# Kernel tuning notes

Measured on AMD Instinct MI355X. Metric: run time of the kernel, lower is better.

Reference implementation:

```python
import jax, jax.numpy as jnp
import numpy as np

SR = 48000
SOUND_SPEED = 343.0
MAX_ORDER = 10
RIR_LEN = 24000
BETA = 0.9          # uniform wall reflection coefficient
TAPS = 81           # fractional-delay windowed-sinc length
HALF = TAPS // 2    # 40 taps each side; also the global RIR offset


def _axis_tables(max_order):
    # Allen-Berkley image indices per axis: coord = (1-2p)*src + 2n*L
    n = np.arange(-max_order, max_order + 1)            # [2N+1]
    p = np.array([0, 1])
    P, N = np.meshgrid(p, n, indexing='ij')             # [2, 2N+1]
    sign = (1 - 2 * P).ravel().astype(np.float32)       # +/-1
    off = (2 * N).ravel().astype(np.float32)
    order = (np.abs(N - P) + np.abs(N)).ravel().astype(np.float32)  # wall hits per axis
    return jnp.asarray(sign), jnp.asarray(off), jnp.asarray(order)  # each [42]


def setup_inputs() -> dict:
    key = jax.random.key(0)
    # fractions in (0.1, 0.9): avoids degenerate rooms / mic-on-wall
    x = 0.1 + 0.8 * jax.random.uniform(key, (8, 9), dtype=jnp.float32)
    return {"input": x}


def reference(input):
    room = input[:, 0:3] * 10.0                 # [B,3] room dimensions (m)
    mic = input[:, 3:6] * room                  # [B,3]
    src = input[:, 6:9] * room                  # [B,3]
    B = room.shape[0]

    sign, off, order = _axis_tables(MAX_ORDER)  # [A] each, A=42

    # per-axis image coordinate minus mic coordinate: [B,3,A]
    img = sign[None, None, :] * src[:, :, None] + off[None, None, :] * room[:, :, None]
    d = img - mic[:, :, None]

    # squared distance over 3-axis outer product -> [B,A,A,A] -> [B,I], I=A^3
    d2 = (d[:, 0, :, None, None] ** 2
          + d[:, 1, None, :, None] ** 2
          + d[:, 2, None, None, :] ** 2)
    dist = jnp.sqrt(d2).reshape(B, -1)                              # [B,I]

    tot_order = (order[:, None, None] + order[None, :, None]
                 + order[None, None, :]).reshape(-1)                # [I]
    keep = tot_order <= MAX_ORDER

    amp = jnp.where(keep[None, :],
                    (BETA ** tot_order)[None, :] / (4.0 * jnp.pi * dist),
                    0.0)                                            # [B,I]

    tau = SR * dist / SOUND_SPEED          # fractional delay in samples
    i0 = jnp.floor(tau)
    frac = tau - i0                        # [B,I] in [0,1)

    k = jnp.arange(TAPS, dtype=jnp.float32) - HALF                   # [T]
    t = k[None, None, :] - frac[:, :, None]                          # [B,I,T]
    win = jnp.where(jnp.abs(t) <= HALF,
                    0.5 * (1.0 + jnp.cos(jnp.pi * t / (HALF + 1))), 0.0)
    h = jnp.sinc(t) * win                                            # windowed sinc

    ki = jnp.arange(TAPS, dtype=jnp.int32)
    idx = i0.astype(jnp.int32)[:, :, None] + HALF + ki[None, None, :]  # [B,I,T]
    valid = (idx >= 0) & (idx < RIR_LEN)
    vals = amp[:, :, None] * h * valid

    bofs = (jnp.arange(B, dtype=jnp.int32) * RIR_LEN)[:, None, None]
    flat_idx = jnp.clip(idx, 0, RIR_LEN - 1) + bofs
    rir = (jnp.zeros(B * RIR_LEN, dtype=jnp.float32)
           .at[flat_idx.ravel()].add(vals.ravel())
           .reshape(B, RIR_LEN))

    origin = 40.0 + SR * jnp.linalg.norm(mic - src, axis=1) / SOUND_SPEED
    return rir, origin
```

## Files before the change

### kernel.cpp

```cpp
#include <hip/hip_runtime.h>
#include <math.h>

#define SRf 48000.0f
#define CSOUND 343.0f
#define RIR_LEN 24000
#define TAPS 81
#define HALFT 40
#define NB 8
#define NM 21
#define NTRIP (NM * NM * NM)
#define NSL 16
#define BLOCK 1024
#define CAPS 256

__device__ __constant__ float c_beta[11] = {
    1.0f, 0.9f, 0.81f, 0.729f, 0.6561f, 0.59049f, 0.531441f,
    0.4782969f, 0.43046721f, 0.387420489f, 0.3486784401f};

__device__ __forceinline__ void axis_entry(int m, float& sgn, float& off, int& ord) {
    if (m < 11) {
        int n = m - 5;
        sgn = 1.0f;
        off = 2.0f * (float)n;
        ord = 2 * abs(n);
    } else {
        int n = m - 15;
        sgn = -1.0f;
        off = 2.0f * (float)n;
        ord = abs(n - 1) + abs(n);
    }
}

__global__ __launch_bounds__(BLOCK) void k_paint(const float* __restrict__ x,
                                                 float* __restrict__ ws) {
    __shared__ __align__(16) float s_tile[RIR_LEN];
    __shared__ float4 s_e[CAPS];
    __shared__ int s_cnt;

    const float PIF = 3.14159265358979323846f;
    const int b = blockIdx.x >> 4;
    const int sl = blockIdx.x & (NSL - 1);
    const int tid = threadIdx.x;

    const float* xb = x + b * 9;
    const float r0 = xb[0] * 10.0f, r1 = xb[1] * 10.0f, r2 = xb[2] * 10.0f;
    const float m0 = xb[3] * r0, m1 = xb[4] * r1, m2 = xb[5] * r2;
    const float s0 = xb[6] * r0, s1 = xb[7] * r1, s2 = xb[8] * r2;

    if (tid == 0) s_cnt = 0;
    for (int j = tid * 4; j < RIR_LEN; j += BLOCK * 4)
        *(float4*)&s_tile[j] = make_float4(0.f, 0.f, 0.f, 0.f);
    __syncthreads();

    {
        int r = sl + tid * NSL;
        if (r < NTRIP) {
            int mi = r / (NM * NM);
            int rem = r - mi * (NM * NM);
            int mj = rem / NM;
            int mk = rem - mj * NM;

            float si, oi_; int qi; axis_entry(mi, si, oi_, qi);
            float sj, oj_; int qj; axis_entry(mj, sj, oj_, qj);
            float sk, ok_; int qk; axis_entry(mk, sk, ok_, qk);
            int q = qi + qj + qk;
            if (q <= 10) {
                float dx = si * s0 + oi_ * r0 - m0;
                float dy = sj * s1 + oj_ * r1 - m1;
                float dz = sk * s2 + ok_ * r2 - m2;
                float dist = sqrtf(dx * dx + dy * dy + dz * dz);

                float tau = SRf * dist / CSOUND;
                float i0f = floorf(tau);
                int i0 = (int)i0f;
                if (i0 + HALFT + 1 < RIR_LEN) {
                    float fr = tau - i0f;
                    float amp = c_beta[q] / (4.0f * PIF * dist);
                    int slot = atomicAdd(&s_cnt, 1);
                    float4 e;
                    e.x = amp;
                    e.y = fr;
                    e.z = amp * __sinf(PIF * fr) * (1.0f / PIF);
                    e.w = __int_as_float(i0);
                    s_e[slot] = e;
                }
            }
        }
    }
    __syncthreads();

    const int n = s_cnt;
    const int total = n * (TAPS - 1);
    for (int w = tid; w < total; w += BLOCK) {
        int img = w / (TAPS - 1);
        int ki = w - img * (TAPS - 1) + 1;
        float4 e = s_e[img];
        int idx = __float_as_int(e.w) + HALFT + ki;
        if (idx >= RIR_LEN) continue;

        float tt = (float)(ki - HALFT) - e.y;
        float win = 0.5f * (1.0f + __cosf(PIF * (1.0f / 41.0f) * tt));
        float v = ((ki & 1) ? e.z : -e.z) * __builtin_amdgcn_rcpf(tt);
        v = (tt == 0.0f) ? e.x : v;
        atomicAdd(&s_tile[idx], v * win);
    }
    __syncthreads();

    float* wb = ws + (size_t)(b * NSL + sl) * RIR_LEN;
    for (int j = tid * 4; j < RIR_LEN; j += BLOCK * 4)
        *(float4*)&wb[j] = *(const float4*)&s_tile[j];
}

__global__ __launch_bounds__(256) void k_reduce(const float* __restrict__ x,
                                                const float* __restrict__ ws,
                                                float* __restrict__ out) {
    int t4 = (blockIdx.x * 256 + threadIdx.x) * 4;
    if (t4 < NB * RIR_LEN) {
        int b = t4 / RIR_LEN;
        int j = t4 - b * RIR_LEN;
        const float* base = ws + (size_t)b * NSL * RIR_LEN + j;
        float4 acc = *(const float4*)base;
        #pragma unroll
        for (int s = 1; s < NSL; ++s) {
            float4 v = *(const float4*)(base + (size_t)s * RIR_LEN);
            acc.x += v.x; acc.y += v.y; acc.z += v.z; acc.w += v.w;
        }
        *(float4*)(out + t4) = acc;
    }
    if (blockIdx.x == 0 && threadIdx.x < NB) {
        const float* xb = x + threadIdx.x * 9;
        float r0 = xb[0] * 10.0f, r1 = xb[1] * 10.0f, r2 = xb[2] * 10.0f;
        float d0 = (xb[3] - xb[6]) * r0;
        float d1 = (xb[4] - xb[7]) * r1;
        float d2 = (xb[5] - xb[8]) * r2;
        float dist = sqrtf(d0 * d0 + d1 * d1 + d2 * d2);
        out[NB * RIR_LEN + threadIdx.x] = 40.0f + SRf * dist / CSOUND;
    }
}

extern "C" void kernel_launch(void* const* d_in, const int* in_sizes, int n_in,
                              void* d_out, int out_size, void* d_ws, size_t ws_size,
                              hipStream_t stream) {
    const float* x = (const float*)d_in[0];
    float* out = (float*)d_out;
    float* ws = (float*)d_ws;

    k_paint<<<NB * NSL, BLOCK, 0, stream>>>(x, ws);
    int rblocks = (NB * RIR_LEN / 4 + 255) / 256;
    k_reduce<<<rblocks, 256, 0, stream>>>(x, ws, out);
}
```

Measured before the change: 26.39 us.

## Fuse paint and reduce kernels via cooperative grid sync

Merges the per-slice painting kernel and the cross-slice reduction kernel into one cooperative kernel that uses a grid-wide barrier between phases. Each block then reduces a 1500-sample span of its batch's RIR across the 16 slice partials. This removes the second kernel launch and its gap. In exchange it pays for a grid barrier and cooperative-launch overhead, and it limits reduction parallelism to 128 blocks.

```diff
diff --git a/kernel.cpp b/kernel.cpp
--- a/kernel.cpp
+++ b/kernel.cpp
@@ -1,4 +1,5 @@
 #include <hip/hip_runtime.h>
+#include <hip/hip_cooperative_groups.h>
 #include <math.h>
 
 #define SRf 48000.0f
@@ -12,6 +13,9 @@
 #define NSL 16
 #define BLOCK 1024
 #define CAPS 256
+#define SPAN (RIR_LEN / NSL)
+
+namespace cg = cooperative_groups;
 
 __device__ __constant__ float c_beta[11] = {
     1.0f, 0.9f, 0.81f, 0.729f, 0.6561f, 0.59049f, 0.531441f,
@@ -31,8 +35,9 @@
     }
 }
 
-__global__ __launch_bounds__(BLOCK) void k_paint(const float* __restrict__ x,
-                                                 float* __restrict__ ws) {
+__global__ __launch_bounds__(BLOCK) void k_fused(const float* __restrict__ x,
+                                                 float* __restrict__ ws,
+                                                 float* __restrict__ out) {
     __shared__ __align__(16) float s_tile[RIR_LEN];
     __shared__ float4 s_e[CAPS];
     __shared__ int s_cnt;
@@ -109,32 +114,30 @@
     float* wb = ws + (size_t)(b * NSL + sl) * RIR_LEN;
     for (int j = tid * 4; j < RIR_LEN; j += BLOCK * 4)
         *(float4*)&wb[j] = *(const float4*)&s_tile[j];
-}
 
-__global__ __launch_bounds__(256) void k_reduce(const float* __restrict__ x,
-                                                const float* __restrict__ ws,
-                                                float* __restrict__ out) {
-    int t4 = (blockIdx.x * 256 + threadIdx.x) * 4;
-    if (t4 < NB * RIR_LEN) {
-        int b = t4 / RIR_LEN;
-        int j = t4 - b * RIR_LEN;
-        const float* base = ws + (size_t)b * NSL * RIR_LEN + j;
-        float4 acc = *(const float4*)base;
-        #pragma unroll
-        for (int s = 1; s < NSL; ++s) {
-            float4 v = *(const float4*)(base + (size_t)s * RIR_LEN);
-            acc.x += v.x; acc.y += v.y; acc.z += v.z; acc.w += v.w;
+    cg::this_grid().sync();
+
+    {
+        int j4 = sl * SPAN + tid * 4;
+        if (tid * 4 < SPAN) {
+            const float* base = ws + (size_t)b * NSL * RIR_LEN + j4;
+            float4 acc = *(const float4*)base;
+            #pragma unroll
+            for (int s = 1; s < NSL; ++s) {
+                float4 v = *(const float4*)(base + (size_t)s * RIR_LEN);
+                acc.x += v.x; acc.y += v.y; acc.z += v.z; acc.w += v.w;
+            }
+            *(float4*)(out + (size_t)b * RIR_LEN + j4) = acc;
         }
-        *(float4*)(out + t4) = acc;
-    }
-    if (blockIdx.x == 0 && threadIdx.x < NB) {
-        const float* xb = x + threadIdx.x * 9;
-        float r0 = xb[0] * 10.0f, r1 = xb[1] * 10.0f, r2 = xb[2] * 10.0f;
-        float d0 = (xb[3] - xb[6]) * r0;
-        float d1 = (xb[4] - xb[7]) * r1;
-        float d2 = (xb[5] - xb[8]) * r2;
-        float dist = sqrtf(d0 * d0 + d1 * d1 + d2 * d2);
-        out[NB * RIR_LEN + threadIdx.x] = 40.0f + SRf * dist / CSOUND;
+        if (blockIdx.x == 0 && tid < NB) {
+            const float* xo = x + tid * 9;
+            float q0 = xo[0] * 10.0f, q1 = xo[1] * 10.0f, q2 = xo[2] * 10.0f;
+            float d0 = (xo[3] - xo[6]) * q0;
+            float d1 = (xo[4] - xo[7]) * q1;
+            float d2 = (xo[5] - xo[8]) * q2;
+            float dist = sqrtf(d0 * d0 + d1 * d1 + d2 * d2);
+            out[NB * RIR_LEN + tid] = 40.0f + SRf * dist / CSOUND;
+        }
     }
 }
 
@@ -145,7 +148,7 @@
     float* out = (float*)d_out;
     float* ws = (float*)d_ws;
 
-    k_paint<<<NB * NSL, BLOCK, 0, stream>>>(x, ws);
-    int rblocks = (NB * RIR_LEN / 4 + 255) / 256;
-    k_reduce<<<rblocks, 256, 0, stream>>>(x, ws, out);
+    void* args[] = {(void*)&x, (void*)&ws, (void*)&out};
+    hipLaunchCooperativeKernel((void*)k_fused, dim3(NB * NSL), dim3(BLOCK),
+                               args, 0, stream);
 }
```

Result: slower. 56.36 us (+113.6%).
